# Kernel optimization log

Measured on AMD Instinct MI355X. Metric: run time of the kernel, lower is better.

The kernel has to match this reference:

```python
import jax, jax.numpy as jnp
import numpy as np

B, T, I, H, K = 8192, 128, 64, 256, 12
KM_ITERS = 25  # fixed iteration count replacing torch's host-synced convergence loop
EPS = 1e-20


def setup_inputs() -> dict:
    key = jax.random.key(0)
    ks = jax.random.split(key, 14)
    s = 1.0 / np.sqrt(H)
    u = lambda k, shape: jax.random.uniform(k, shape, jnp.float32, -s, s)
    return {
        "x": jax.random.normal(ks[0], (B, T, I), jnp.float32),
        "gru_wih": u(ks[1], (3 * H, I)),
        "gru_whh": u(ks[2], (3 * H, H)),
        "gru_bih": u(ks[3], (3 * H,)),
        "gru_bhh": u(ks[4], (3 * H,)),
        "gcn1_w": u(ks[5], (H, H)),
        "gcn1_b": u(ks[6], (H,)),
        "gcn2_w": u(ks[7], (H, H)),
        "gcn2_b": u(ks[8], (H,)),
        "w1_w": u(ks[9], (H, 1)),
        "w1_b": u(ks[10], (1,)),
        "w2_w": u(ks[11], (H, 1)),
        "w2_b": u(ks[12], (1,)),
    }


def _gru_last_hidden(x, wih, whh, bih, bhh):
    # torch nn.GRU math; returns final hidden state [B, H]
    xp = jnp.einsum("bti,gi->tbg", x, wih) + bih  # [T, B, 3H], precompute input proj
    def step(h, xt):
        gh = h @ whh.T + bhh
        xr, xz, xn = jnp.split(xt, 3, axis=-1)
        hr, hz, hn = jnp.split(gh, 3, axis=-1)
        r = jax.nn.sigmoid(xr + hr)
        z = jax.nn.sigmoid(xz + hz)
        n = jnp.tanh(xn + r * hn)
        return (1.0 - z) * n + z * h, None
    h0 = jnp.zeros((x.shape[0], whh.shape[1]), x.dtype)
    h, _ = jax.lax.scan(step, h0, xp)
    return h


def _assign(data, centers):
    # cdist^2 + argmin, as in compute_codes
    d2 = (jnp.sum(data ** 2, axis=1, keepdims=True)
          - 2.0 * data @ centers.T
          + jnp.sum(centers ** 2, axis=1)[None, :])
    return jnp.argmin(d2, axis=1)


def _update_centers(data, codes):
    centers = jax.ops.segment_sum(data, codes, num_segments=K)
    cnt = jax.ops.segment_sum(jnp.ones((data.shape[0],), data.dtype), codes, num_segments=K)
    cnt = jnp.where(cnt > 0.5, cnt, 1.0)
    return centers / cnt[:, None]


def _kmeans(data):
    # codes are non-differentiable (argmin); final centers differentiable via scatter_add
    d = jax.lax.stop_gradient(data)
    idx = jax.random.choice(jax.random.key(7), d.shape[0], (K,), replace=False)
    codes = _assign(d, d[idx])
    def step(codes, _):
        return _assign(d, _update_centers(d, codes)), None
    codes, _ = jax.lax.scan(step, codes, None, length=KM_ITERS)
    centers = _update_centers(data, codes)  # grads flow through last update only, as in torch
    return centers, codes


def reference(x, gru_wih, gru_whh, gru_bih, gru_bhh,
              gcn1_w, gcn1_b, gcn2_w, gcn2_b, w1_w, w1_b, w2_w, w2_b):
    hidden = _gru_last_hidden(x, gru_wih, gru_whh, gru_bih, gru_bhh)  # [B, H]
    centers, _codes = _kmeans(hidden)                                  # [K, H]
    adj = jnp.eye(K, dtype=hidden.dtype)  # A_mat is None -> identity adjacency
    e = jax.nn.relu(hidden @ centers.T)   # [B, K]
    # straight-through gumbel softmax, temperature 1, hard=True
    U = jax.random.uniform(jax.random.key(42), e.shape, e.dtype)
    g = -jnp.log(-jnp.log(U + EPS) + EPS)
    y = jax.nn.softmax(e + g, axis=-1)
    y_hard = jax.nn.one_hot(jnp.argmax(y, axis=-1), K, dtype=y.dtype)
    scores = jax.lax.stop_gradient(y_hard - y) + y
    # two GCN layers over centers
    h1 = jax.nn.relu(adj @ (centers @ gcn1_w) + gcn1_b)
    h2 = jax.nn.relu(adj @ (h1 @ gcn2_w) + gcn2_b)
    clu = scores @ h2                     # [B, H]
    wa = jax.nn.sigmoid(clu @ w1_w + w1_b)
    wb = jax.nn.sigmoid(hidden @ w2_w + w2_b)
    wa = wa / (wa + wb)
    out = wa * clu + (1.0 - wa) * hidden  # dropout is a no-op in eval mode
    return out
```

## Files before the change

kernel.cpp:

```cpp
#include <hip/hip_runtime.h>
#include <hip/hip_bf16.h>
#include <stdint.h>

#define BN 8192
#define TT 128
#define II 64
#define HH 256
#define GG 768
#define KK 12
#define KM_ITERS_N 25
#define UB 64
#define UPB (BN/UB)
#define KSTEPS 20

typedef __attribute__((ext_vector_type(8))) _Float16 f16x8;
typedef __attribute__((ext_vector_type(4))) _Float16 f16x4;
typedef __attribute__((ext_vector_type(16))) float f32x16;

__device__ __forceinline__ uint32_t rotl32(uint32_t v, int d) {
  return (v << d) | (v >> (32 - d));
}
__device__ __forceinline__ void tf2x32(uint32_t k0, uint32_t k1,
                                       uint32_t x0, uint32_t x1,
                                       uint32_t& o0, uint32_t& o1) {
  uint32_t ks2 = k0 ^ k1 ^ 0x1BD11BDAu;
  x0 += k0; x1 += k1;
#define TFR(r) { x0 += x1; x1 = rotl32(x1, r); x1 ^= x0; }
  TFR(13); TFR(15); TFR(26); TFR(6);   x0 += k1;  x1 += ks2 + 1u;
  TFR(17); TFR(29); TFR(16); TFR(24);  x0 += ks2; x1 += k0 + 2u;
  TFR(13); TFR(15); TFR(26); TFR(6);   x0 += k0;  x1 += k1 + 3u;
  TFR(17); TFR(29); TFR(16); TFR(24);  x0 += k1;  x1 += ks2 + 4u;
  TFR(13); TFR(15); TFR(26); TFR(6);   x0 += ks2; x1 += k0 + 5u;
#undef TFR
  o0 = x0; o1 = x1;
}
__device__ __forceinline__ float bits_to_unit(uint32_t bits) {
  uint32_t u = (bits >> 9) | 0x3f800000u;
  return __uint_as_float(u) - 1.0f;
}

#define RSCL 4096.f
#define RINV (1.f / 4096.f)
__device__ __forceinline__ void split2h(float v, _Float16& m, _Float16& r) {
  m = (_Float16)v;
  r = (_Float16)((v - (float)m) * RSCL);
}

__device__ __forceinline__ float sigm_f(float u) {
  return 1.f / (1.f + exp2f(u * -1.4426950408889634f));
}
__device__ __forceinline__ float tanh_f(float u) {
  return 1.f - 2.f / (1.f + exp2f(u * 2.8853900817779268f));
}

__global__ void k_pack4(const float* __restrict__ wih, const float* __restrict__ whh,
                        char* __restrict__ wpk4) {
  int u = blockIdx.x * 256 + threadIdx.x;
  if (u >= KSTEPS * 24 * 2 * 64) return;
  int lane = u & 63; int rest = u >> 6;
  int p = rest & 1; rest >>= 1;
  int cf = rest % 24; int ks = rest / 24;
  int l31 = lane & 31, khalf = lane >> 5;
  int col = cf * 32 + l31;
  int gate = col >> 8, d = col & 255;
  int grow = gate * 256 + d;
  _Float16 s[8];
#pragma unroll
  for (int j = 0; j < 8; ++j) {
    int k = khalf * 8 + j;
    float wv = (ks < 4) ? wih[grow * II + ks * 16 + k]
                        : whh[grow * HH + (ks - 4) * 16 + k];
    _Float16 m, r;
    split2h(wv, m, r);
    s[j] = p ? r : m;
  }
  *(f16x8*)(wpk4 + (size_t)u * 16) = *(f16x8*)s;
}

#define GLHS 260
#define GLB 40960

__global__ __launch_bounds__(512, 2) void k_gru_v8(
    const float* __restrict__ x, const char* __restrict__ wpk4,
    const float* __restrict__ bih, const float* __restrict__ bhh,
    float* __restrict__ hf_out) {
  __shared__ __align__(16) char smem[74240];
  float* glh = (float*)(smem + GLB);
  const int tid = threadIdx.x;
  const int w = tid >> 6;
  const int l = tid & 63, l31 = l & 31, kh5 = l >> 5;
  const int row0 = blockIdx.x * 32;

  {
    int4 z = {0, 0, 0, 0};
    int4* s4 = (int4*)smem;
#pragma unroll
    for (int i = 0; i < 4; ++i) s4[tid + i * 512] = z;
    for (int i = tid; i < 32 * GLHS; i += 512) glh[i] = 0.f;
  }
  const int d = w * 32 + l31;
  const float biR = bih[d],          bhR = bhh[d];
  const float biZ = bih[HH + d],     bhZ = bhh[HH + d];
  const float biN = bih[2 * HH + d], bhN = bhh[2 * HH + d];

  const int xrow = tid & 31, xko4 = tid >> 5;
  const float* xbase = x + (size_t)(row0 + xrow) * (TT * II) + xko4 * 4;
  float4 xreg = *(const float4*)xbase;
  __syncthreads();

#define FRAG3(ACCM, ACCR, CF, KS)                                                  \
    {                                                                              \
      const char* bf = wpk4 + (((size_t)(KS) * 24 + (CF)) * 2) * 1024 +            \
                       (size_t)l * 16;                                             \
      f16x8 b0 = *(const f16x8*)(bf);                                              \
      f16x8 b1 = *(const f16x8*)(bf + 1024);                                       \
      ACCM = __builtin_amdgcn_mfma_f32_32x32x16_f16(a0, b0, ACCM, 0, 0, 0);        \
      ACCR = __builtin_amdgcn_mfma_f32_32x32x16_f16(a0, b1, ACCR, 0, 0, 0);        \
      ACCR = __builtin_amdgcn_mfma_f32_32x32x16_f16(a1, b0, ACCR, 0, 0, 0);        \
    }

  for (int t = 0; t < TT; ++t) {
    {
      _Float16 m[4], r[4];
      split2h(xreg.x, m[0], r[0]);
      split2h(xreg.y, m[1], r[1]);
      split2h(xreg.z, m[2], r[2]);
      split2h(xreg.w, m[3], r[3]);
      int xks = xko4 >> 2, kh = (xko4 >> 1) & 1, sub = (xko4 & 1) * 8;
      char* b0 = smem + 32768 + (size_t)(xks * 4 + kh) * 512 + xrow * 16 + sub;
      *(f16x4*)b0 = *(f16x4*)m;
      *(f16x4*)(b0 + 1024) = *(f16x4*)r;
    }
    if (t + 1 < TT) xreg = *(const float4*)(xbase + (size_t)(t + 1) * II);
    __syncthreads();

    f32x16 rrv, zzv;
    {
      f32x16 aRm = (f32x16)0.f, aRr = (f32x16)0.f;
      f32x16 aZm = (f32x16)0.f, aZr = (f32x16)0.f;
#pragma unroll
      for (int ks = 0; ks < 4; ++ks) {
        const char* ab = smem + 32768 + (size_t)(ks * 4 + kh5) * 512 + l31 * 16;
        f16x8 a0 = *(const f16x8*)(ab);
        f16x8 a1 = *(const f16x8*)(ab + 1024);
        FRAG3(aRm, aRr, w, ks) FRAG3(aZm, aZr, 8 + w, ks)
      }
#pragma unroll 4
      for (int ks = 4; ks < KSTEPS; ++ks) {
        const char* ab = smem + (size_t)((ks - 4) * 4 + kh5) * 512 + l31 * 16;
        f16x8 a0 = *(const f16x8*)(ab);
        f16x8 a1 = *(const f16x8*)(ab + 1024);
        FRAG3(aRm, aRr, w, ks) FRAG3(aZm, aZr, 8 + w, ks)
      }
#pragma unroll
      for (int j = 0; j < 16; ++j) {
        rrv[j] = sigm_f(aRm[j] + aRr[j] * RINV + biR + bhR);
        zzv[j] = sigm_f(aZm[j] + aZr[j] * RINV + biZ + bhZ);
      }
    }
    f32x16 aNxm = (f32x16)0.f, aNxr = (f32x16)0.f;
    f32x16 aNhm = (f32x16)0.f, aNhr = (f32x16)0.f;
#pragma unroll
    for (int ks = 0; ks < 4; ++ks) {
      const char* ab = smem + 32768 + (size_t)(ks * 4 + kh5) * 512 + l31 * 16;
      f16x8 a0 = *(const f16x8*)(ab);
      f16x8 a1 = *(const f16x8*)(ab + 1024);
      FRAG3(aNxm, aNxr, 16 + w, ks)
    }
#pragma unroll 4
    for (int ks = 4; ks < KSTEPS; ++ks) {
      const char* ab = smem + (size_t)((ks - 4) * 4 + kh5) * 512 + l31 * 16;
      f16x8 a0 = *(const f16x8*)(ab);
      f16x8 a1 = *(const f16x8*)(ab + 1024);
      FRAG3(aNhm, aNhr, 16 + w, ks)
    }
    __syncthreads();

    const bool lastT = (t == TT - 1);
#pragma unroll
    for (int j = 0; j < 16; ++j) {
      int row = (j & 3) + ((j >> 2) << 3) + kh5 * 4;
      float hold = glh[row * GLHS + d];
      float Nx = aNxm[j] + aNxr[j] * RINV;
      float Nh = aNhm[j] + aNhr[j] * RINV;
      float nn = tanh_f(Nx + biN + rrv[j] * (Nh + bhN));
      float hnew = (1.f - zzv[j]) * nn + zzv[j] * hold;
      glh[row * GLHS + d] = hnew;
      if (lastT) hf_out[(size_t)(row0 + row) * HH + d] = hnew;
    }
    __syncthreads();

    if (!lastT) {
#pragma unroll
      for (int i = 0; i < 2; ++i) {
        int u = tid + i * 512;
        int prow = u & 31, kunit = u >> 5;
        const float* gsrc = glh + prow * GLHS + kunit * 8;
        float4 v0 = *(const float4*)(gsrc);
        float4 v1 = *(const float4*)(gsrc + 4);
        _Float16 m[8], r[8];
        split2h(v0.x, m[0], r[0]); split2h(v0.y, m[1], r[1]);
        split2h(v0.z, m[2], r[2]); split2h(v0.w, m[3], r[3]);
        split2h(v1.x, m[4], r[4]); split2h(v1.y, m[5], r[5]);
        split2h(v1.z, m[6], r[6]); split2h(v1.w, m[7], r[7]);
        int hks = kunit >> 1, kh = kunit & 1;
        char* basep = smem + (size_t)(hks * 4 + kh) * 512 + prow * 16;
        *(f16x8*)(basep) = *(f16x8*)m;
        *(f16x8*)(basep + 1024) = *(f16x8*)r;
      }
    }
  }
#undef FRAG3
}

__global__ void k_prng_setup(uint32_t* sk) {
  uint32_t k0, k1, s0, s1, t0, t1;
  tf2x32(0u, 7u, 0u, 0u, k0, k1);
  tf2x32(0u, 7u, 0u, 1u, s0, s1);
  tf2x32(k0, k1, 0u, 1u, t0, t1);
  sk[0] = s0; sk[1] = s1;
  sk[2] = t0; sk[3] = t1;
}

__global__ void k_genkeys(const uint32_t* __restrict__ sk, int which,
                          uint32_t* __restrict__ keys) {
  int i = blockIdx.x * blockDim.x + threadIdx.x;
  if (i < BN) {
    uint32_t o0, o1;
    tf2x32(sk[which * 2], sk[which * 2 + 1], 0u, (uint32_t)i, o0, o1);
    keys[i] = o0 ^ o1;
  }
}

#define RSE 16
__global__ __launch_bounds__(256) void k_ranksort(const uint32_t* __restrict__ keys,
                                                  const int* __restrict__ vin,
                                                  int* __restrict__ vout) {
  __shared__ uint32_t skey[BN];
  __shared__ int psum[RSE][17];
  const int tid = threadIdx.x;
  const int g = tid >> 4;
  const int l = tid & 15;
  const int gi = blockIdx.x * RSE + g;
  for (int i = tid; i < BN; i += 256) skey[i] = keys[i];
  __syncthreads();
  const uint32_t ki = skey[gi];
  int rank = 0;
#pragma unroll 8
  for (int j = l; j < BN; j += 16) {
    uint32_t kj = skey[j];
    rank += (kj < ki) || (kj == ki && j < gi);
  }
  psum[g][l] = rank;
  __syncthreads();
  if (l == 0) {
    int r = 0;
#pragma unroll
    for (int tt = 0; tt < 16; ++tt) r += psum[g][tt];
    vout[r] = vin ? vin[gi] : gi;
  }
}

__global__ void k_init_centers(const float* __restrict__ h, const int* __restrict__ vals2,
                               float* __restrict__ centers, double* __restrict__ cnorm) {
  const int c = blockIdx.x, d = threadIdx.x;
  const int src = vals2[c];
  float v = h[(size_t)src * HH + d];
  centers[c * HH + d] = v;
  __shared__ double red[HH];
  red[d] = (double)v * (double)v;
  __syncthreads();
  for (int s = 128; s > 0; s >>= 1) {
    if (d < s) red[d] += red[d + s];
    __syncthreads();
  }
  if (d == 0) cnorm[c] = red[0];
}

__global__ __launch_bounds__(128) void k_assign(const float* __restrict__ h,
                                                const float* __restrict__ centers,
                                                const double* __restrict__ cnorm,
                                                int* __restrict__ codes) {
  __shared__ float sc[KK * HH];
  __shared__ double sn[KK];
  const int tid = threadIdx.x;
  for (int idx = tid; idx < KK * HH; idx += 128) sc[idx] = centers[idx];
  if (tid < KK) sn[tid] = cnorm[tid];
  __syncthreads();
  const int gid = blockIdx.x * 128 + tid;
  const int b = gid >> 1, half = gid & 1;
  const float4* hp = (const float4*)&h[(size_t)b * HH + half * 128];
  const float* sch = sc + half * 128;
  double acc[KK] = {};
  double xn = 0.0;
  for (int k4 = 0; k4 < 32; ++k4) {
    float4 xv = hp[k4];
    double x0 = xv.x, x1 = xv.y, x2 = xv.z, x3 = xv.w;
    xn += x0 * x0 + x1 * x1 + x2 * x2 + x3 * x3;
#pragma unroll
    for (int c = 0; c < KK; ++c) {
      float4 cv = *(const float4*)&sch[c * HH + k4 * 4];
      acc[c] += x0 * cv.x + x1 * cv.y + x2 * cv.z + x3 * cv.w;
    }
  }
  xn += __shfl_xor(xn, 1);
#pragma unroll
  for (int c = 0; c < KK; ++c) acc[c] += __shfl_xor(acc[c], 1);
  if (half == 0) {
    int best = 0;
    double bd = xn - 2.0 * acc[0] + sn[0];
#pragma unroll
    for (int c = 1; c < KK; ++c) {
      double d2 = xn - 2.0 * acc[c] + sn[c];
      if (d2 < bd) { bd = d2; best = c; }
    }
    codes[b] = best;
  }
}

__global__ __launch_bounds__(256) void k_upd_partial(const float* __restrict__ h,
                                                     const int* __restrict__ codes,
                                                     double* __restrict__ psum,
                                                     float* __restrict__ pcnt) {
  __shared__ double acc[KK * HH];
  __shared__ int lc[UPB];
  const int tid = threadIdx.x;
  for (int idx = tid; idx < KK * HH; idx += 256) acc[idx] = 0.0;
  const int p0 = blockIdx.x * UPB;
  for (int idx = tid; idx < UPB; idx += 256) lc[idx] = codes[p0 + idx];
  __syncthreads();
  const int d = tid;
  for (int p = 0; p < UPB; ++p) {
    int c = lc[p];
    acc[c * HH + d] += (double)h[(size_t)(p0 + p) * HH + d];
  }
  if (tid < KK) {
    float cnt = 0.f;
    for (int p = 0; p < UPB; ++p) cnt += (lc[p] == tid) ? 1.f : 0.f;
    pcnt[blockIdx.x * KK + tid] = cnt;
  }
  for (int c = 0; c < KK; ++c)
    psum[((size_t)blockIdx.x * KK + c) * HH + d] = acc[c * HH + d];
}

__global__ void k_upd_final(const double* __restrict__ psum, const float* __restrict__ pcnt,
                            float* __restrict__ centers, double* __restrict__ cnorm) {
  const int c = blockIdx.x, d = threadIdx.x;
  double s = 0.0;
  for (int b = 0; b < UB; ++b) s += psum[((size_t)b * KK + c) * HH + d];
  float cnt = 0.f;
  for (int b = 0; b < UB; ++b) cnt += pcnt[b * KK + c];
  if (cnt <= 0.5f) cnt = 1.f;
  float v = (float)(s / (double)cnt);
  centers[c * HH + d] = v;
  __shared__ double red[HH];
  red[d] = (double)v * (double)v;
  __syncthreads();
  for (int s2 = 128; s2 > 0; s2 >>= 1) {
    if (d < s2) red[d] += red[d + s2];
    __syncthreads();
  }
  if (d == 0) cnorm[c] = red[0];
}

__global__ __launch_bounds__(128) void k_gumbel(const float* __restrict__ h,
                                                const float* __restrict__ centers,
                                                int* __restrict__ codeg) {
  __shared__ float sc[KK * HH];
  const int tid = threadIdx.x;
  for (int idx = tid; idx < KK * HH; idx += 128) sc[idx] = centers[idx];
  __syncthreads();
  const int b = blockIdx.x * 128 + tid;
  const float4* hp = (const float4*)&h[(size_t)b * HH];
  double acc[KK] = {};
  for (int k4 = 0; k4 < HH / 4; ++k4) {
    float4 xv = hp[k4];
    double x0 = xv.x, x1 = xv.y, x2 = xv.z, x3 = xv.w;
#pragma unroll
    for (int c = 0; c < KK; ++c) {
      float4 cv = *(const float4*)&sc[c * HH + k4 * 4];
      acc[c] += x0 * cv.x + x1 * cv.y + x2 * cv.z + x3 * cv.w;
    }
  }
  int best = 0;
  double bv = -1e300;
#pragma unroll
  for (int c = 0; c < KK; ++c) {
    double e = acc[c] > 0.0 ? acc[c] : 0.0;
    uint32_t j = (uint32_t)(b * KK + c);
    uint32_t o0, o1;
    tf2x32(0u, 42u, 0u, j, o0, o1);
    double U = (double)bits_to_unit(o0 ^ o1);
    double g = -log(-log(U + 1e-20) + 1e-20);
    double v = e + g;
    if (v > bv) { bv = v; best = c; }
  }
  codeg[b] = best;
}

__global__ void k_gcn(const float* __restrict__ in, const float* __restrict__ w,
                      const float* __restrict__ bias, float* __restrict__ out) {
  const int c = blockIdx.x, d = threadIdx.x;
  __shared__ float si[HH];
  si[d] = in[c * HH + d];
  __syncthreads();
  float acc = 0.f;
  for (int k = 0; k < HH; ++k) acc += si[k] * w[k * HH + d];
  acc += bias[d];
  out[c * HH + d] = acc > 0.f ? acc : 0.f;
}

__global__ __launch_bounds__(256) void k_final(const float* __restrict__ h,
                                               const float* __restrict__ h2,
                                               const int* __restrict__ codeg,
                                               const float* __restrict__ w1,
                                               const float* __restrict__ w1b,
                                               const float* __restrict__ w2,
                                               const float* __restrict__ w2b,
                                               float* __restrict__ out) {
  const int b = blockIdx.x, d = threadIdx.x;
  const int cg = codeg[b];
  const float cd = h2[cg * HH + d];
  const float hd = h[(size_t)b * HH + d];
  __shared__ float r1[HH], r2[HH];
  __shared__ float wan_s;
  r1[d] = cd * w1[d];
  r2[d] = hd * w2[d];
  __syncthreads();
  for (int s = 128; s > 0; s >>= 1) {
    if (d < s) { r1[d] += r1[d + s]; r2[d] += r2[d + s]; }
    __syncthreads();
  }
  if (d == 0) {
    float wa = 1.f / (1.f + expf(-(r1[0] + w1b[0])));
    float wb = 1.f / (1.f + expf(-(r2[0] + w2b[0])));
    wan_s = wa / (wa + wb);
  }
  __syncthreads();
  float wan = wan_s;
  out[(size_t)b * HH + d] = wan * cd + (1.f - wan) * hd;
}

extern "C" void kernel_launch(void* const* d_in, const int* in_sizes, int n_in,
                              void* d_out, int out_size, void* d_ws, size_t ws_size,
                              hipStream_t stream) {
  const float* x   = (const float*)d_in[0];
  const float* wih = (const float*)d_in[1];
  const float* whh = (const float*)d_in[2];
  const float* bih = (const float*)d_in[3];
  const float* bhh = (const float*)d_in[4];
  const float* g1w = (const float*)d_in[5];
  const float* g1b = (const float*)d_in[6];
  const float* g2w = (const float*)d_in[7];
  const float* g2b = (const float*)d_in[8];
  const float* w1w = (const float*)d_in[9];
  const float* w1b = (const float*)d_in[10];
  const float* w2w = (const float*)d_in[11];
  const float* w2b = (const float*)d_in[12];
  float* out = (float*)d_out;

  char* wsb = (char*)d_ws;
  size_t off = 0;
  auto alloc = [&](size_t bytes) {
    void* p = wsb + off;
    off += (bytes + 255) & ~(size_t)255;
    return p;
  };
  float* hf0      = (float*)alloc((size_t)BN * HH * 4);
  char*  wpk4     = (char*)alloc((size_t)KSTEPS * 24 * 2 * 64 * 16);
  float* centers  = (float*)alloc(KK * HH * 4);
  double* cnorm   = (double*)alloc(KK * 8);
  int*   codes    = (int*)alloc(BN * 4);
  int*   codeg    = (int*)alloc(BN * 4);
  uint32_t* keys  = (uint32_t*)alloc(BN * 4);
  int*   vals1    = (int*)alloc(BN * 4);
  int*   vals2    = (int*)alloc(BN * 4);
  uint32_t* sk    = (uint32_t*)alloc(4 * 4);
  double* psum    = (double*)alloc((size_t)UB * KK * HH * 8);
  float* pcnt     = (float*)alloc(UB * KK * 4);
  float* hh1      = (float*)alloc(KK * HH * 4);
  float* hh2      = (float*)alloc(KK * HH * 4);

  k_pack4<<<(KSTEPS * 24 * 2 * 64 + 255) / 256, 256, 0, stream>>>(wih, whh, wpk4);
  k_gru_v8<<<BN / 32, 512, 0, stream>>>(x, wpk4, bih, bhh, hf0);
  float* h = hf0;

  k_prng_setup<<<1, 1, 0, stream>>>(sk);
  k_genkeys<<<32, 256, 0, stream>>>(sk, 0, keys);
  k_ranksort<<<BN / RSE, 256, 0, stream>>>(keys, (const int*)nullptr, vals1);
  k_genkeys<<<32, 256, 0, stream>>>(sk, 1, keys);
  k_ranksort<<<BN / RSE, 256, 0, stream>>>(keys, vals1, vals2);

  k_init_centers<<<KK, HH, 0, stream>>>(h, vals2, centers, cnorm);
  k_assign<<<BN * 2 / 128, 128, 0, stream>>>(h, centers, cnorm, codes);
  for (int it = 0; it < KM_ITERS_N; ++it) {
    k_upd_partial<<<UB, 256, 0, stream>>>(h, codes, psum, pcnt);
    k_upd_final<<<KK, HH, 0, stream>>>(psum, pcnt, centers, cnorm);
    k_assign<<<BN * 2 / 128, 128, 0, stream>>>(h, centers, cnorm, codes);
  }
  k_upd_partial<<<UB, 256, 0, stream>>>(h, codes, psum, pcnt);
  k_upd_final<<<KK, HH, 0, stream>>>(psum, pcnt, centers, cnorm);

  k_gumbel<<<BN / 128, 128, 0, stream>>>(h, centers, codeg);
  k_gcn<<<KK, HH, 0, stream>>>(centers, g1w, g1b, hh1);
  k_gcn<<<KK, HH, 0, stream>>>(hh1, g2w, g2b, hh2);
  k_final<<<BN, HH, 0, stream>>>(h, hh2, codeg, w1w, w1b, w2w, w2b, out);
}
```

Baseline: 3.880 ms.

## Split GRU recurrence K-dimension across two wave halves with LDS reduction

The GRU kernel moves to 1024 threads per block. Sixteen waves are split into two halves that each compute part of the K range (x plus the first 6 h-steps versus the remaining 10 h-steps) for the same output columns, and partial sums are combined through new LDS scratch buffers. The goal is to shorten the per-timestep serial MFMA chain on the latency-bound recurrence. The cost is extra barriers and scratch traffic, a much larger LDS footprint, and one block per CU instead of two.

```diff
diff --git a/kernel.cpp b/kernel.cpp
--- a/kernel.cpp
+++ b/kernel.cpp
@@ -79,15 +79,17 @@
 
 #define GLHS 260
 #define GLB 40960
-
-__global__ __launch_bounds__(512, 2) void k_gru_v8(
+#define SCRB 74240
+
+__global__ __launch_bounds__(1024, 1) void k_gru_v9(
     const float* __restrict__ x, const char* __restrict__ wpk4,
     const float* __restrict__ bih, const float* __restrict__ bhh,
     float* __restrict__ hf_out) {
-  __shared__ __align__(16) char smem[74240];
+  __shared__ __align__(16) char smem[139776];
   float* glh = (float*)(smem + GLB);
   const int tid = threadIdx.x;
   const int w = tid >> 6;
+  const int wg = w & 7, half = w >> 3;
   const int l = tid & 63, l31 = l & 31, kh5 = l >> 5;
   const int row0 = blockIdx.x * 32;
 
@@ -95,18 +97,22 @@
     int4 z = {0, 0, 0, 0};
     int4* s4 = (int4*)smem;
 #pragma unroll
-    for (int i = 0; i < 4; ++i) s4[tid + i * 512] = z;
-    for (int i = tid; i < 32 * GLHS; i += 512) glh[i] = 0.f;
-  }
-  const int d = w * 32 + l31;
+    for (int i = 0; i < 2; ++i) s4[tid + i * 1024] = z;
+    for (int i = tid; i < 32 * GLHS; i += 1024) glh[i] = 0.f;
+  }
+  const int d = wg * 32 + l31;
   const float biR = bih[d],          bhR = bhh[d];
   const float biZ = bih[HH + d],     bhZ = bhh[HH + d];
   const float biN = bih[2 * HH + d], bhN = bhh[2 * HH + d];
 
-  const int xrow = tid & 31, xko4 = tid >> 5;
+  const int xrow = tid & 31, xko4 = (tid >> 5) & 15;
   const float* xbase = x + (size_t)(row0 + xrow) * (TT * II) + xko4 * 4;
-  float4 xreg = *(const float4*)xbase;
-  __syncthreads();
+  float4 xreg;
+  if (tid < 512) xreg = *(const float4*)xbase;
+  __syncthreads();
+
+  float* scrA = (float*)(smem + SCRB);
+  float* scrB = (float*)(smem + SCRB + 32768);
 
 #define FRAG3(ACCM, ACCR, CF, KS)                                                  \
     {                                                                              \
@@ -118,9 +124,11 @@
       ACCR = __builtin_amdgcn_mfma_f32_32x32x16_f16(a0, b1, ACCR, 0, 0, 0);        \
       ACCR = __builtin_amdgcn_mfma_f32_32x32x16_f16(a1, b0, ACCR, 0, 0, 0);        \
     }
+#define XADDR(KS) (smem + 32768 + (size_t)((KS) * 4 + kh5) * 512 + l31 * 16)
+#define HADDR(KS) (smem + (size_t)(((KS) - 4) * 4 + kh5) * 512 + l31 * 16)
 
   for (int t = 0; t < TT; ++t) {
-    {
+    if (tid < 512) {
       _Float16 m[4], r[4];
       split2h(xreg.x, m[0], r[0]);
       split2h(xreg.y, m[1], r[1]);
@@ -130,87 +138,129 @@
       char* b0 = smem + 32768 + (size_t)(xks * 4 + kh) * 512 + xrow * 16 + sub;
       *(f16x4*)b0 = *(f16x4*)m;
       *(f16x4*)(b0 + 1024) = *(f16x4*)r;
-    }
-    if (t + 1 < TT) xreg = *(const float4*)(xbase + (size_t)(t + 1) * II);
+      if (t + 1 < TT) xreg = *(const float4*)(xbase + (size_t)(t + 1) * II);
+    }
     __syncthreads();
 
     f32x16 rrv, zzv;
     {
       f32x16 aRm = (f32x16)0.f, aRr = (f32x16)0.f;
       f32x16 aZm = (f32x16)0.f, aZr = (f32x16)0.f;
+      if (half == 0) {
+#pragma unroll
+        for (int ks = 0; ks < 4; ++ks) {
+          const char* ab = XADDR(ks);
+          f16x8 a0 = *(const f16x8*)(ab);
+          f16x8 a1 = *(const f16x8*)(ab + 1024);
+          FRAG3(aRm, aRr, wg, ks) FRAG3(aZm, aZr, 8 + wg, ks)
+        }
+#pragma unroll
+        for (int ks = 4; ks < 10; ++ks) {
+          const char* ab = HADDR(ks);
+          f16x8 a0 = *(const f16x8*)(ab);
+          f16x8 a1 = *(const f16x8*)(ab + 1024);
+          FRAG3(aRm, aRr, wg, ks) FRAG3(aZm, aZr, 8 + wg, ks)
+        }
+      } else {
+#pragma unroll
+        for (int ks = 10; ks < KSTEPS; ++ks) {
+          const char* ab = HADDR(ks);
+          f16x8 a0 = *(const f16x8*)(ab);
+          f16x8 a1 = *(const f16x8*)(ab + 1024);
+          FRAG3(aRm, aRr, wg, ks) FRAG3(aZm, aZr, 8 + wg, ks)
+        }
+      }
+      if (half == 1) {
+#pragma unroll
+        for (int j = 0; j < 16; ++j) {
+          int row = (j & 3) + ((j >> 2) << 3) + kh5 * 4;
+          scrA[wg * 1024 + row * 32 + l31] = aRm[j] + aRr[j] * RINV;
+          scrB[wg * 1024 + row * 32 + l31] = aZm[j] + aZr[j] * RINV;
+        }
+      }
+      __syncthreads();
+      if (half == 0) {
+#pragma unroll
+        for (int j = 0; j < 16; ++j) {
+          int row = (j & 3) + ((j >> 2) << 3) + kh5 * 4;
+          float Rc = aRm[j] + aRr[j] * RINV + scrA[wg * 1024 + row * 32 + l31];
+          float Zc = aZm[j] + aZr[j] * RINV + scrB[wg * 1024 + row * 32 + l31];
+          rrv[j] = sigm_f(Rc + biR + bhR);
+          zzv[j] = sigm_f(Zc + biZ + bhZ);
+        }
+      }
+    }
+    f32x16 aNxm = (f32x16)0.f, aNxr = (f32x16)0.f;
+    f32x16 aNhm = (f32x16)0.f, aNhr = (f32x16)0.f;
+    if (half == 0) {
 #pragma unroll
       for (int ks = 0; ks < 4; ++ks) {
-        const char* ab = smem + 32768 + (size_t)(ks * 4 + kh5) * 512 + l31 * 16;
+        const char* ab = XADDR(ks);
         f16x8 a0 = *(const f16x8*)(ab);
         f16x8 a1 = *(const f16x8*)(ab + 1024);
-        FRAG3(aRm, aRr, w, ks) FRAG3(aZm, aZr, 8 + w, ks)
-      }
-#pragma unroll 4
-      for (int ks = 4; ks < KSTEPS; ++ks) {
-        const char* ab = smem + (size_t)((ks - 4) * 4 + kh5) * 512 + l31 * 16;
+        FRAG3(aNxm, aNxr, 16 + wg, ks)
+      }
+#pragma unroll
+      for (int ks = 4; ks < 10; ++ks) {
+        const char* ab = HADDR(ks);
         f16x8 a0 = *(const f16x8*)(ab);
         f16x8 a1 = *(const f16x8*)(ab + 1024);
-        FRAG3(aRm, aRr, w, ks) FRAG3(aZm, aZr, 8 + w, ks)
-      }
+        FRAG3(aNhm, aNhr, 16 + wg, ks)
+      }
+    } else {
+#pragma unroll
+      for (int ks = 10; ks < KSTEPS; ++ks) {
+        const char* ab = HADDR(ks);
+        f16x8 a0 = *(const f16x8*)(ab);
+        f16x8 a1 = *(const f16x8*)(ab + 1024);
+        FRAG3(aNhm, aNhr, 16 + wg, ks)
+      }
+    }
+    __syncthreads();
+    if (half == 1) {
 #pragma unroll
       for (int j = 0; j < 16; ++j) {
-        rrv[j] = sigm_f(aRm[j] + aRr[j] * RINV + biR + bhR);
-        zzv[j] = sigm_f(aZm[j] + aZr[j] * RINV + biZ + bhZ);
-      }
-    }
-    f32x16 aNxm = (f32x16)0.f, aNxr = (f32x16)0.f;
-    f32x16 aNhm = (f32x16)0.f, aNhr = (f32x16)0.f;
-#pragma unroll
-    for (int ks = 0; ks < 4; ++ks) {
-      const char* ab = smem + 32768 + (size_t)(ks * 4 + kh5) * 512 + l31 * 16;
-      f16x8 a0 = *(const f16x8*)(ab);
-      f16x8 a1 = *(const f16x8*)(ab + 1024);
-      FRAG3(aNxm, aNxr, 16 + w, ks)
-    }
-#pragma unroll 4
-    for (int ks = 4; ks < KSTEPS; ++ks) {
-      const char* ab = smem + (size_t)((ks - 4) * 4 + kh5) * 512 + l31 * 16;
-      f16x8 a0 = *(const f16x8*)(ab);
-      f16x8 a1 = *(const f16x8*)(ab + 1024);
-      FRAG3(aNhm, aNhr, 16 + w, ks)
+        int row = (j & 3) + ((j >> 2) << 3) + kh5 * 4;
+        scrA[wg * 1024 + row * 32 + l31] = aNhm[j] + aNhr[j] * RINV;
+      }
     }
     __syncthreads();
 
     const bool lastT = (t == TT - 1);
-#pragma unroll
-    for (int j = 0; j < 16; ++j) {
-      int row = (j & 3) + ((j >> 2) << 3) + kh5 * 4;
-      float hold = glh[row * GLHS + d];
-      float Nx = aNxm[j] + aNxr[j] * RINV;
-      float Nh = aNhm[j] + aNhr[j] * RINV;
-      float nn = tanh_f(Nx + biN + rrv[j] * (Nh + bhN));
-      float hnew = (1.f - zzv[j]) * nn + zzv[j] * hold;
-      glh[row * GLHS + d] = hnew;
-      if (lastT) hf_out[(size_t)(row0 + row) * HH + d] = hnew;
+    if (half == 0) {
+#pragma unroll
+      for (int j = 0; j < 16; ++j) {
+        int row = (j & 3) + ((j >> 2) << 3) + kh5 * 4;
+        float hold = glh[row * GLHS + d];
+        float Nx = aNxm[j] + aNxr[j] * RINV;
+        float Nh = aNhm[j] + aNhr[j] * RINV + scrA[wg * 1024 + row * 32 + l31];
+        float nn = tanh_f(Nx + biN + rrv[j] * (Nh + bhN));
+        float hnew = (1.f - zzv[j]) * nn + zzv[j] * hold;
+        glh[row * GLHS + d] = hnew;
+        if (lastT) hf_out[(size_t)(row0 + row) * HH + d] = hnew;
+      }
     }
     __syncthreads();
 
     if (!lastT) {
-#pragma unroll
-      for (int i = 0; i < 2; ++i) {
-        int u = tid + i * 512;
-        int prow = u & 31, kunit = u >> 5;
-        const float* gsrc = glh + prow * GLHS + kunit * 8;
-        float4 v0 = *(const float4*)(gsrc);
-        float4 v1 = *(const float4*)(gsrc + 4);
-        _Float16 m[8], r[8];
-        split2h(v0.x, m[0], r[0]); split2h(v0.y, m[1], r[1]);
-        split2h(v0.z, m[2], r[2]); split2h(v0.w, m[3], r[3]);
-        split2h(v1.x, m[4], r[4]); split2h(v1.y, m[5], r[5]);
-        split2h(v1.z, m[6], r[6]); split2h(v1.w, m[7], r[7]);
-        int hks = kunit >> 1, kh = kunit & 1;
-        char* basep = smem + (size_t)(hks * 4 + kh) * 512 + prow * 16;
-        *(f16x8*)(basep) = *(f16x8*)m;
-        *(f16x8*)(basep + 1024) = *(f16x8*)r;
-      }
+      int prow = tid & 31, kunit = tid >> 5;
+      const float* gsrc = glh + prow * GLHS + kunit * 8;
+      float4 v0 = *(const float4*)(gsrc);
+      float4 v1 = *(const float4*)(gsrc + 4);
+      _Float16 m[8], r[8];
+      split2h(v0.x, m[0], r[0]); split2h(v0.y, m[1], r[1]);
+      split2h(v0.z, m[2], r[2]); split2h(v0.w, m[3], r[3]);
+      split2h(v1.x, m[4], r[4]); split2h(v1.y, m[5], r[5]);
+      split2h(v1.z, m[6], r[6]); split2h(v1.w, m[7], r[7]);
+      int hks = kunit >> 1, kh = kunit & 1;
+      char* basep = smem + (size_t)(hks * 4 + kh) * 512 + prow * 16;
+      *(f16x8*)(basep) = *(f16x8*)m;
+      *(f16x8*)(basep + 1024) = *(f16x8*)r;
     }
   }
 #undef FRAG3
+#undef XADDR
+#undef HADDR
 }
 
 __global__ void k_prng_setup(uint32_t* sk) {
@@ -482,7 +532,7 @@
   float* hh2      = (float*)alloc(KK * HH * 4);
 
   k_pack4<<<(KSTEPS * 24 * 2 * 64 + 255) / 256, 256, 0, stream>>>(wih, whh, wpk4);
-  k_gru_v8<<<BN / 32, 512, 0, stream>>>(x, wpk4, bih, bhh, hf0);
+  k_gru_v9<<<BN / 32, 1024, 0, stream>>>(x, wpk4, bih, bhh, hf0);
   float* h = hf0;
 
   k_prng_setup<<<1, 1, 0, stream>>>(sk);
```

After: 8.383 ms. 116% more time.

## Fuse k-means assignment with partial center accumulation in one kernel

Applied to the files above, without the earlier changes.

Merges the per-row nearest-center assignment and the per-block partial sum/count accumulation into a single kernel, `k_fa`. Each 256-thread block handles 32 rows: eight threads per row compute the distances and reduce them with shuffles, then the block accumulates the row sums into shared memory. This drops one launch per k-means iteration and removes the global round trip of the codes array. In exchange there are 256 partial buffers instead of 64, so the 12-block final reduction must read four times as much double-precision partial data. Each block also uses more shared memory, which limits occupancy.

```diff
diff --git a/kernel.cpp b/kernel.cpp
--- a/kernel.cpp
+++ b/kernel.cpp
@@ -9,9 +9,9 @@
 #define GG 768
 #define KK 12
 #define KM_ITERS_N 25
-#define UB 64
-#define UPB (BN/UB)
 #define KSTEPS 20
+#define FAB 32
+#define NPART (BN/FAB)
 
 typedef __attribute__((ext_vector_type(8))) _Float16 f16x8;
 typedef __attribute__((ext_vector_type(4))) _Float16 f16x4;
@@ -277,66 +277,61 @@
   if (d == 0) cnorm[c] = red[0];
 }
 
-__global__ __launch_bounds__(128) void k_assign(const float* __restrict__ h,
-                                                const float* __restrict__ centers,
-                                                const double* __restrict__ cnorm,
-                                                int* __restrict__ codes) {
+__global__ __launch_bounds__(256) void k_fa(const float* __restrict__ h,
+                                            const float* __restrict__ centers,
+                                            const double* __restrict__ cnorm,
+                                            double* __restrict__ psum,
+                                            float* __restrict__ pcnt) {
   __shared__ float sc[KK * HH];
   __shared__ double sn[KK];
+  __shared__ int lcode[FAB];
+  __shared__ double acc[KK * HH];
   const int tid = threadIdx.x;
-  for (int idx = tid; idx < KK * HH; idx += 128) sc[idx] = centers[idx];
+  for (int i = tid; i < KK * HH; i += 256) { sc[i] = centers[i]; acc[i] = 0.0; }
   if (tid < KK) sn[tid] = cnorm[tid];
   __syncthreads();
-  const int gid = blockIdx.x * 128 + tid;
-  const int b = gid >> 1, half = gid & 1;
-  const float4* hp = (const float4*)&h[(size_t)b * HH + half * 128];
-  const float* sch = sc + half * 128;
-  double acc[KK] = {};
+  const int row0 = blockIdx.x * FAB;
+  const int r = tid >> 3, seg = tid & 7;
+  const int grow = row0 + r;
+  const float4* hp = (const float4*)&h[(size_t)grow * HH + seg * 32];
+  const float* schp = sc + seg * 32;
+  double dot[KK] = {};
   double xn = 0.0;
-  for (int k4 = 0; k4 < 32; ++k4) {
+#pragma unroll
+  for (int k4 = 0; k4 < 8; ++k4) {
     float4 xv = hp[k4];
     double x0 = xv.x, x1 = xv.y, x2 = xv.z, x3 = xv.w;
     xn += x0 * x0 + x1 * x1 + x2 * x2 + x3 * x3;
 #pragma unroll
     for (int c = 0; c < KK; ++c) {
-      float4 cv = *(const float4*)&sch[c * HH + k4 * 4];
-      acc[c] += x0 * cv.x + x1 * cv.y + x2 * cv.z + x3 * cv.w;
-    }
-  }
-  xn += __shfl_xor(xn, 1);
-#pragma unroll
-  for (int c = 0; c < KK; ++c) acc[c] += __shfl_xor(acc[c], 1);
-  if (half == 0) {
+      float4 cv = *(const float4*)&schp[c * HH + k4 * 4];
+      dot[c] += x0 * cv.x + x1 * cv.y + x2 * cv.z + x3 * cv.w;
+    }
+  }
+  xn += __shfl_xor(xn, 1); xn += __shfl_xor(xn, 2); xn += __shfl_xor(xn, 4);
+#pragma unroll
+  for (int c = 0; c < KK; ++c) {
+    dot[c] += __shfl_xor(dot[c], 1);
+    dot[c] += __shfl_xor(dot[c], 2);
+    dot[c] += __shfl_xor(dot[c], 4);
+  }
+  if (seg == 0) {
     int best = 0;
-    double bd = xn - 2.0 * acc[0] + sn[0];
+    double bd = xn - 2.0 * dot[0] + sn[0];
 #pragma unroll
     for (int c = 1; c < KK; ++c) {
-      double d2 = xn - 2.0 * acc[c] + sn[c];
+      double d2 = xn - 2.0 * dot[c] + sn[c];
       if (d2 < bd) { bd = d2; best = c; }
     }
-    codes[b] = best;
-  }
-}
-
-__global__ __launch_bounds__(256) void k_upd_partial(const float* __restrict__ h,
-                                                     const int* __restrict__ codes,
-                                                     double* __restrict__ psum,
-                                                     float* __restrict__ pcnt) {
-  __shared__ double acc[KK * HH];
-  __shared__ int lc[UPB];
-  const int tid = threadIdx.x;
-  for (int idx = tid; idx < KK * HH; idx += 256) acc[idx] = 0.0;
-  const int p0 = blockIdx.x * UPB;
-  for (int idx = tid; idx < UPB; idx += 256) lc[idx] = codes[p0 + idx];
+    lcode[r] = best;
+  }
   __syncthreads();
   const int d = tid;
-  for (int p = 0; p < UPB; ++p) {
-    int c = lc[p];
-    acc[c * HH + d] += (double)h[(size_t)(p0 + p) * HH + d];
-  }
+  for (int p = 0; p < FAB; ++p)
+    acc[lcode[p] * HH + d] += (double)h[(size_t)(row0 + p) * HH + d];
   if (tid < KK) {
     float cnt = 0.f;
-    for (int p = 0; p < UPB; ++p) cnt += (lc[p] == tid) ? 1.f : 0.f;
+    for (int p = 0; p < FAB; ++p) cnt += (lcode[p] == tid) ? 1.f : 0.f;
     pcnt[blockIdx.x * KK + tid] = cnt;
   }
   for (int c = 0; c < KK; ++c)
@@ -347,9 +342,9 @@
                             float* __restrict__ centers, double* __restrict__ cnorm) {
   const int c = blockIdx.x, d = threadIdx.x;
   double s = 0.0;
-  for (int b = 0; b < UB; ++b) s += psum[((size_t)b * KK + c) * HH + d];
+  for (int b = 0; b < NPART; ++b) s += psum[((size_t)b * KK + c) * HH + d];
   float cnt = 0.f;
-  for (int b = 0; b < UB; ++b) cnt += pcnt[b * KK + c];
+  for (int b = 0; b < NPART; ++b) cnt += pcnt[b * KK + c];
   if (cnt <= 0.5f) cnt = 1.f;
   float v = (float)(s / (double)cnt);
   centers[c * HH + d] = v;
@@ -470,14 +465,13 @@
   char*  wpk4     = (char*)alloc((size_t)KSTEPS * 24 * 2 * 64 * 16);
   float* centers  = (float*)alloc(KK * HH * 4);
   double* cnorm   = (double*)alloc(KK * 8);
-  int*   codes    = (int*)alloc(BN * 4);
   int*   codeg    = (int*)alloc(BN * 4);
   uint32_t* keys  = (uint32_t*)alloc(BN * 4);
   int*   vals1    = (int*)alloc(BN * 4);
   int*   vals2    = (int*)alloc(BN * 4);
   uint32_t* sk    = (uint32_t*)alloc(4 * 4);
-  double* psum    = (double*)alloc((size_t)UB * KK * HH * 8);
-  float* pcnt     = (float*)alloc(UB * KK * 4);
+  double* psum    = (double*)alloc((size_t)NPART * KK * HH * 8);
+  float* pcnt     = (float*)alloc(NPART * KK * 4);
   float* hh1      = (float*)alloc(KK * HH * 4);
   float* hh2      = (float*)alloc(KK * HH * 4);
 
@@ -492,13 +486,11 @@
   k_ranksort<<<BN / RSE, 256, 0, stream>>>(keys, vals1, vals2);
 
   k_init_centers<<<KK, HH, 0, stream>>>(h, vals2, centers, cnorm);
-  k_assign<<<BN * 2 / 128, 128, 0, stream>>>(h, centers, cnorm, codes);
+  k_fa<<<NPART, 256, 0, stream>>>(h, centers, cnorm, psum, pcnt);
   for (int it = 0; it < KM_ITERS_N; ++it) {
-    k_upd_partial<<<UB, 256, 0, stream>>>(h, codes, psum, pcnt);
     k_upd_final<<<KK, HH, 0, stream>>>(psum, pcnt, centers, cnorm);
-    k_assign<<<BN * 2 / 128, 128, 0, stream>>>(h, centers, cnorm, codes);
-  }
-  k_upd_partial<<<UB, 256, 0, stream>>>(h, codes, psum, pcnt);
+    k_fa<<<NPART, 256, 0, stream>>>(h, centers, cnorm, psum, pcnt);
+  }
   k_upd_final<<<KK, HH, 0, stream>>>(psum, pcnt, centers, cnorm);
 
   k_gumbel<<<BN / 128, 128, 0, stream>>>(h, centers, codeg);
```

Measured after the change: 3.820 ms. No clear change (-1.5%).
